# Kernel optimization log

Hardware: AMD Instinct MI355X
Metric: run time of the kernel (lower is better)

The kernel has to match this reference:

```python
import jax, jax.numpy as jnp
import numpy as np

PH = PW = 7          # pooled output size
SR = 2               # sampling_ratio: SR x SR samples per bin
SCALES = (0.25, 0.125, 0.0625, 0.03125)  # FPN strides 4,8,16,32
K = 512              # number of ROIs
B = 2                # batch (images)
IMG = 800.0


def _coords(start, bsize, P):
    # sample coords for P bins, SR samples per bin: start + p*bin + (i+0.5)*bin/SR
    j = jnp.arange(P * SR, dtype=start.dtype)
    return (start[:, None]
            + (j // SR)[None, :] * bsize[:, None]
            + ((j % SR) + 0.5)[None, :] * (bsize[:, None] / SR))  # [K, P*SR]


def _roi_align_level(feat, rois, scale):
    # feat: [B, C, H, W] ; rois: [K, 5] (batch_idx, x1, y1, x2, y2 in image coords)
    Bf, C, H, W = feat.shape
    b = rois[:, 0].astype(jnp.int32)
    x1 = rois[:, 1] * scale
    y1 = rois[:, 2] * scale
    x2 = rois[:, 3] * scale
    y2 = rois[:, 4] * scale
    roi_w = jnp.maximum(x2 - x1, 1.0)   # legacy (aligned=False) ROIAlign
    roi_h = jnp.maximum(y2 - y1, 1.0)
    ys = _coords(y1, roi_h / PH, PH)    # [K, Sy]
    xs = _coords(x1, roi_w / PW, PW)    # [K, Sx]
    y = ys[:, :, None]                  # [K, Sy, 1]
    x = xs[:, None, :]                  # [K, 1, Sx]
    valid = (y > -1.0) & (y < H) & (x > -1.0) & (x < W)  # [K, Sy, Sx]
    yc = jnp.clip(y, 0.0, None)
    xc = jnp.clip(x, 0.0, None)
    yl = jnp.minimum(yc.astype(jnp.int32), H - 1)
    xl = jnp.minimum(xc.astype(jnp.int32), W - 1)
    yh = jnp.minimum(yl + 1, H - 1)
    xh = jnp.minimum(xl + 1, W - 1)
    ly = jnp.where(yl >= H - 1, 0.0, yc - yl)
    lx = jnp.where(xl >= W - 1, 0.0, xc - xl)
    hy, hx = 1.0 - ly, 1.0 - lx
    feat_flat = feat.reshape(Bf, C, H * W)
    Sy, Sx = PH * SR, PW * SR
    acc = jnp.zeros((rois.shape[0], C, Sy, Sx), feat.dtype)
    corners = ((yl, xl, hy * hx), (yl, xh, hy * lx),
               (yh, xl, ly * hx), (yh, xh, ly * lx))
    for yy, xx, w in corners:  # fixed 4-corner loop (not a data-dim loop)
        idx = jnp.broadcast_to(yy * W + xx, (rois.shape[0], Sy, Sx))
        vals = jax.vmap(lambda bi, ii: jnp.take(feat_flat, bi, axis=0)[:, ii])(b, idx)
        acc = acc + vals * jnp.broadcast_to(w, idx.shape)[:, None, :, :]
    acc = jnp.where(valid[:, None, :, :], acc, 0.0)
    # average SRxSR samples within each 7x7 bin
    return acc.reshape(rois.shape[0], C, PH, SR, PW, SR).mean(axis=(3, 5))


def setup_inputs() -> dict:
    key = jax.random.key(0)
    ks = jax.random.split(key, 10)
    input_0 = jax.random.normal(ks[0], (B, 256, 200, 200), jnp.float32)
    input_1 = jax.random.normal(ks[1], (B, 256, 100, 100), jnp.float32)
    input_2 = jax.random.normal(ks[2], (B, 256, 50, 50), jnp.float32)
    input_3 = jax.random.normal(ks[3], (B, 256, 25, 25), jnp.float32)
    bidx = jax.random.randint(ks[4], (K,), 0, B).astype(jnp.float32)
    x1 = jax.random.uniform(ks[5], (K,)) * (IMG - 64.0)
    y1 = jax.random.uniform(ks[6], (K,)) * (IMG - 64.0)
    bw = 32.0 + jax.random.uniform(ks[7], (K,)) * 200.0
    bh = 32.0 + jax.random.uniform(ks[8], (K,)) * 200.0
    rois = jnp.stack([bidx, x1, y1,
                      jnp.minimum(x1 + bw, IMG),
                      jnp.minimum(y1 + bh, IMG)], axis=1).astype(jnp.float32)
    level = jax.random.randint(ks[9], (K,), 0, 4).astype(jnp.int32)
    rois_counts = jnp.array([K // 2, K - K // 2], jnp.int32)  # unused (all ROIs valid)
    return {"input_0": input_0, "input_1": input_1, "input_2": input_2,
            "input_3": input_3, "rois": rois, "rois_counts": rois_counts,
            "level": level}


def reference(input_0, input_1, input_2, input_3, rois, rois_counts, level):
    feats = (input_0, input_1, input_2, input_3)
    lvl = level.astype(jnp.int32)
    out = jnp.zeros((rois.shape[0], input_0.shape[1], PH, PW), input_0.dtype)
    for i, (f, s) in enumerate(zip(feats, SCALES)):
        o = _roi_align_level(f, rois, s)
        out = out + jnp.where((lvl == i)[:, None, None, None], o, 0.0)
    return out
```

## Files before the change

### kernel.cpp

```cpp
#include <hip/hip_runtime.h>


#define NUM_CH 256
#define CGRP   64
#define OFF2   5120000
#define OFF3   6400000
#define WS_FLOATS 6720000
#define TBLK_FULL 1400

typedef float floatx2 __attribute__((ext_vector_type(2)));
typedef float floatx4 __attribute__((ext_vector_type(4)));

__device__ __forceinline__ float ext4(floatx4 v, int i) {
    float r = (i == 1) ? v.y : v.x;
    r = (i == 2) ? v.z : r;
    r = (i == 3) ? v.w : r;
    return r;
}

template<int H, int W, int P>
__device__ __forceinline__ void transpose_row(
    const float* __restrict__ src, float* __restrict__ dst, int m, float* lds)
{
    int b  = m / (H * 4);
    int rm = m - b * (H * 4);
    int y  = rm >> 2;
    int ct = rm & 3;
    int tid = threadIdx.x;
    const float* s = src + (((size_t)b * NUM_CH + ct * 64) * H + y) * W;
    for (int i = tid; i < 64 * W; i += 256) {
        int c = i / W;
        int x = i - c * W;
        lds[c * P + x] = s[(size_t)c * (H * W) + x];
    }
    __syncthreads();
    float* d = dst + (((size_t)b * H + y) * (size_t)W) * NUM_CH + ct * 64;
    for (int i = tid; i < W * 64; i += 256) {
        int x = i >> 6;
        int c = i & 63;
        d[(size_t)x * NUM_CH + c] = lds[c * P + x];
    }
}

__global__ __launch_bounds__(256) void k1_transpose_gather(
    const float* __restrict__ f0,
    const float* __restrict__ f1,
    const float* __restrict__ f2,
    const float* __restrict__ f3,
    const float* __restrict__ rois_f,
    const int* __restrict__ level,
    float* __restrict__ out,
    float* __restrict__ ws,
    int K, int TBLK, int all_levels)
{
    __shared__ float lds[64 * 101];
    int bid = blockIdx.x;
    if (bid < TBLK) {
        if (bid < 800)       transpose_row<100, 100, 101>(f1, ws,        bid,        lds);
        else if (bid < 1200) transpose_row<50,  50,  51 >(f2, ws + OFF2, bid - 800,  lds);
        else                 transpose_row<25,  25,  27 >(f3, ws + OFF3, bid - 1200, lds);
        return;
    }

    int nb  = gridDim.x - TBLK;
    int lb  = bid - TBLK;
    int q   = nb >> 3, r = nb & 7;
    int xcd = lb & 7;
    int idx = lb >> 3;
    int l   = xcd * q + min(xcd, r) + idx;

    int NW  = K * CGRP;
    int wid = l * 4 + (int)(threadIdx.x >> 6);
    if (wid >= NW) return;
    int lane = threadIdx.x & 63;
    if (lane >= 49) return;

    int k  = wid % K;
    int c2 = wid / K;
    k  = __builtin_amdgcn_readfirstlane(k);
    c2 = __builtin_amdgcn_readfirstlane(c2);

    int lvl = level[k];
    if (!all_levels && lvl != 0) return;

    const float* f;
    int H, W; float scale;
    if (lvl == 0)      { f = f0; H = 200; W = 200; scale = 0.25f;    }
    else if (lvl == 1) { f = f1; H = 100; W = 100; scale = 0.125f;   }
    else if (lvl == 2) { f = f2; H = 50;  W = 50;  scale = 0.0625f;  }
    else               { f = f3; H = 25;  W = 25;  scale = 0.03125f; }

    int p  = lane;
    int ph = p / 7;
    int pw = p % 7;

    const float* rf = rois_f + (size_t)k * 5;
    float r0 = rf[0];
    float x1 = rf[1] * scale, y1 = rf[2] * scale;
    float x2 = rf[3] * scale, y2 = rf[4] * scale;
    int bi = (int)r0;
    bi = (bi < 0) ? 0 : ((bi > 1) ? 1 : bi);

    float bh = fmaxf(y2 - y1, 1.0f) * (1.0f / 7.0f);
    float bw = fmaxf(x2 - x1, 1.0f) * (1.0f / 7.0f);

    const size_t plane = (size_t)(H * W);
    const float* base  = f + ((size_t)bi * NUM_CH + c2) * plane;
    const size_t cstr  = (size_t)CGRP * plane;

    int   rA[2], rB[2];
    float lyv[2], hyv[2], vy[2];
    #pragma unroll
    for (int sy = 0; sy < 2; ++sy) {
        float y = y1 + (float)ph * bh + ((float)sy + 0.5f) * (bh * 0.5f);
        bool valid = (y > -1.0f) && (y < (float)H);
        float yc = fmaxf(y, 0.0f);
        int yl = min((int)yc, H - 1);
        int yh = min(yl + 1, H - 1);
        float ly = (yl >= H - 1) ? 0.0f : (yc - (float)yl);
        rA[sy] = yl * W;
        rB[sy] = yh * W;
        lyv[sy] = ly; hyv[sy] = 1.0f - ly;
        vy[sy] = valid ? 0.25f : 0.0f;
    }
    int   xlv[2], xhv[2];
    float lxv[2], hxv[2], vx[2];
    #pragma unroll
    for (int sx = 0; sx < 2; ++sx) {
        float x = x1 + (float)pw * bw + ((float)sx + 0.5f) * (bw * 0.5f);
        bool valid = (x > -1.0f) && (x < (float)W);
        float xc = fmaxf(x, 0.0f);
        int xl = min((int)xc, W - 1);
        float lx = (xl >= W - 1) ? 0.0f : (xc - (float)xl);
        xlv[sx] = xl;
        xhv[sx] = min(xl + 1, W - 1);
        lxv[sx] = lx; hxv[sx] = 1.0f - lx;
        vx[sx] = valid ? 1.0f : 0.0f;
    }

    float acc[4];
    #pragma unroll
    for (int j = 0; j < 4; ++j) acc[j] = 0.0f;

    if (bw <= 3.98f) {
        int xq = min(xlv[0], W - 4);
        int i0l = min(max(xlv[0] - xq, 0), 3);
        int i0h = min(max(xhv[0] - xq, 0), 3);
        int i1l = min(max(xlv[1] - xq, 0), 3);
        int i1h = min(max(xhv[1] - xq, 0), 3);

        #pragma unroll
        for (int sy = 0; sy < 2; ++sy) {
            floatx4 LA[4], LB[4];
            #pragma unroll
            for (int j = 0; j < 4; ++j) {
                const float* bj = base + (size_t)j * cstr;
                LA[j] = *(const floatx4*)(bj + rA[sy] + xq);
                LB[j] = *(const floatx4*)(bj + rB[sy] + xq);
            }
            #pragma unroll
            for (int sx = 0; sx < 2; ++sx) {
                int il = sx ? i1l : i0l;
                int ih = sx ? i1h : i0h;
                float vs  = vy[sy] * vx[sx];
                float w00 = hyv[sy] * hxv[sx] * vs;
                float w01 = hyv[sy] * lxv[sx] * vs;
                float w10 = lyv[sy] * hxv[sx] * vs;
                float w11 = lyv[sy] * lxv[sx] * vs;
                #pragma unroll
                for (int j = 0; j < 4; ++j) {
                    acc[j] += w00 * ext4(LA[j], il) + w01 * ext4(LA[j], ih)
                            + w10 * ext4(LB[j], il) + w11 * ext4(LB[j], ih);
                }
            }
        }
    } else {
        int   xb[2];
        float sel[2];
        #pragma unroll
        for (int sx = 0; sx < 2; ++sx) {
            int xq = min(xlv[sx], W - 2);
            xb[sx]  = xq;
            sel[sx] = (xlv[sx] > xq) ? 1.0f : 0.0f;
        }
        #pragma unroll
        for (int sy = 0; sy < 2; ++sy) {
            floatx2 va[4][2], vb[4][2];
            #pragma unroll
            for (int sx = 0; sx < 2; ++sx) {
                #pragma unroll
                for (int j = 0; j < 4; ++j) {
                    const float* bj = base + (size_t)j * cstr;
                    va[j][sx] = *(const floatx2*)(bj + rA[sy] + xb[sx]);
                    vb[j][sx] = *(const floatx2*)(bj + rB[sy] + xb[sx]);
                }
            }
            #pragma unroll
            for (int sx = 0; sx < 2; ++sx) {
                float vs  = vy[sy] * vx[sx];
                float w00 = hyv[sy] * hxv[sx] * vs;
                float w01 = hyv[sy] * lxv[sx] * vs;
                float w10 = lyv[sy] * hxv[sx] * vs;
                float w11 = lyv[sy] * lxv[sx] * vs;
                float s0  = sel[sx];
                #pragma unroll
                for (int j = 0; j < 4; ++j) {
                    float v00 = va[j][sx].x + s0 * (va[j][sx].y - va[j][sx].x);
                    float v10 = vb[j][sx].x + s0 * (vb[j][sx].y - vb[j][sx].x);
                    acc[j] += w00 * v00 + w01 * va[j][sx].y
                            + w10 * v10 + w11 * vb[j][sx].y;
                }
            }
        }
    }

    size_t ob = ((size_t)k * NUM_CH + c2) * 49 + p;
    #pragma unroll
    for (int j = 0; j < 4; ++j)
        out[ob + (size_t)j * (CGRP * 49)] = acc[j];
}

__global__ __launch_bounds__(256) void k2_gather_l123(
    const float* __restrict__ rois_f,
    const int* __restrict__ level,
    const float* __restrict__ ws,
    float* __restrict__ out,
    int K)
{
    __shared__ float lds[49 * 257];
    int k = blockIdx.x;
    int lvl = level[k];
    if (lvl == 0) return;

    const float* t; int H, W; float scale;
    if (lvl == 1)      { t = ws;        H = 100; W = 100; scale = 0.125f;   }
    else if (lvl == 2) { t = ws + OFF2; H = 50;  W = 50;  scale = 0.0625f;  }
    else               { t = ws + OFF3; H = 25;  W = 25;  scale = 0.03125f; }

    const float* rf = rois_f + (size_t)k * 5;
    float r0 = rf[0];
    float x1 = rf[1] * scale, y1 = rf[2] * scale;
    float x2 = rf[3] * scale, y2 = rf[4] * scale;
    int bi = (int)r0;
    bi = (bi < 0) ? 0 : ((bi > 1) ? 1 : bi);

    float bh = fmaxf(y2 - y1, 1.0f) * (1.0f / 7.0f);
    float bw = fmaxf(x2 - x1, 1.0f) * (1.0f / 7.0f);

    const float* tb = t + (size_t)bi * H * W * NUM_CH;
    int wave = threadIdx.x >> 6;
    int lane = threadIdx.x & 63;
    int cb   = lane * 4;

    for (int px = wave; px < 49; px += 4) {
        int ph = px / 7, pw = px % 7;

        int rows[4]; float lyv[2], hyv[2], vy[2];
        #pragma unroll
        for (int sy = 0; sy < 2; ++sy) {
            float y = y1 + (float)ph * bh + ((float)sy + 0.5f) * (bh * 0.5f);
            bool valid = (y > -1.0f) && (y < (float)H);
            float yc = fmaxf(y, 0.0f);
            int yl = min((int)yc, H - 1);
            int yh = min(yl + 1, H - 1);
            float ly = (yl >= H - 1) ? 0.0f : (yc - (float)yl);
            rows[2 * sy]     = yl;
            rows[2 * sy + 1] = yh;
            lyv[sy] = ly; hyv[sy] = 1.0f - ly;
            vy[sy] = valid ? 0.25f : 0.0f;
        }
        int cols[4]; float lxv[2], hxv[2], vx[2];
        #pragma unroll
        for (int sx = 0; sx < 2; ++sx) {
            float x = x1 + (float)pw * bw + ((float)sx + 0.5f) * (bw * 0.5f);
            bool valid = (x > -1.0f) && (x < (float)W);
            float xc = fmaxf(x, 0.0f);
            int xl = min((int)xc, W - 1);
            float lx = (xl >= W - 1) ? 0.0f : (xc - (float)xl);
            cols[2 * sx]     = xl;
            cols[2 * sx + 1] = min(xl + 1, W - 1);
            lxv[sx] = lx; hxv[sx] = 1.0f - lx;
            vx[sx] = valid ? 1.0f : 0.0f;
        }

        floatx4 v[4][4];
        #pragma unroll
        for (int rr = 0; rr < 4; ++rr) {
            #pragma unroll
            for (int cc = 0; cc < 4; ++cc) {
                v[rr][cc] = *(const floatx4*)(
                    tb + ((size_t)rows[rr] * W + cols[cc]) * NUM_CH + cb);
            }
        }

        floatx4 acc = {0.0f, 0.0f, 0.0f, 0.0f};
        #pragma unroll
        for (int sy = 0; sy < 2; ++sy) {
            #pragma unroll
            for (int sx = 0; sx < 2; ++sx) {
                float vs  = vy[sy] * vx[sx];
                float w00 = hyv[sy] * hxv[sx] * vs;
                float w01 = hyv[sy] * lxv[sx] * vs;
                float w10 = lyv[sy] * hxv[sx] * vs;
                float w11 = lyv[sy] * lxv[sx] * vs;
                acc += v[2 * sy][2 * sx]     * w00;
                acc += v[2 * sy][2 * sx + 1] * w01;
                acc += v[2 * sy + 1][2 * sx]     * w10;
                acc += v[2 * sy + 1][2 * sx + 1] * w11;
            }
        }

        int lb = px * 257 + cb;
        lds[lb + 0] = acc.x;
        lds[lb + 1] = acc.y;
        lds[lb + 2] = acc.z;
        lds[lb + 3] = acc.w;
    }
    __syncthreads();

    float* ob = out + (size_t)k * (NUM_CH * 49);
    for (int i = threadIdx.x; i < NUM_CH * 49; i += 256) {
        int c  = i / 49;
        int px = i - c * 49;
        ob[i] = lds[px * 257 + c];
    }
}

extern "C" void kernel_launch(void* const* d_in, const int* in_sizes, int n_in,
                              void* d_out, int out_size, void* d_ws, size_t ws_size,
                              hipStream_t stream) {
    const float* f0   = (const float*)d_in[0];
    const float* f1   = (const float*)d_in[1];
    const float* f2   = (const float*)d_in[2];
    const float* f3   = (const float*)d_in[3];
    const float* rois = (const float*)d_in[4];
    const int* level = (const int*)d_in[6];
    float* out = (float*)d_out;

    int K = out_size / (NUM_CH * 49);
    int use_ws = (ws_size >= (size_t)WS_FLOATS * 4) ? 1 : 0;
    int TBLK = use_ws ? TBLK_FULL : 0;
    int GB   = K * 16;

    k1_transpose_gather<<<TBLK + GB, 256, 0, stream>>>(
        f0, f1, f2, f3, rois, level, out, (float*)d_ws, K, TBLK, use_ws ? 0 : 1);
    if (use_ws) {
        k2_gather_l123<<<K, 256, 0, stream>>>(
            rois, level, (const float*)d_ws, out, K);
    }
}
```

Before: 192.3 us.

## Transpose level-0 features to channels-last and gather all levels from workspace

```diff
diff --git a/kernel.cpp b/kernel.cpp
--- a/kernel.cpp
+++ b/kernel.cpp
@@ -3,10 +3,13 @@
 
 #define NUM_CH 256
 #define CGRP   64
-#define OFF2   5120000
-#define OFF3   6400000
-#define WS_FLOATS 6720000
-#define TBLK_FULL 1400
+#define OFF_T2 5120000
+#define OFF_T3 6400000
+#define WS_SMALL 6720000
+#define OFF_T0 6720000
+#define WS_FULL 27200000
+#define TBLK13 1400
+#define TBLK0  3200
 
 typedef float floatx2 __attribute__((ext_vector_type(2)));
 typedef float floatx4 __attribute__((ext_vector_type(4)));
@@ -42,31 +45,202 @@
     }
 }
 
-__global__ __launch_bounds__(256) void k1_transpose_gather(
+__device__ __forceinline__ void transpose_l0(
+    const float* __restrict__ src, float* __restrict__ dst, int m, float* lds)
+{
+    int b   = m / 1600;
+    int rm  = m - b * 1600;
+    int y   = rm >> 3;
+    int sub = rm & 7;
+    int ct  = sub >> 1;
+    int xh  = sub & 1;
+    int tid = threadIdx.x;
+    const float* s = src + (((size_t)b * NUM_CH + ct * 64) * 200 + y) * 200
+                         + xh * 100;
+    for (int i = tid; i < 64 * 25; i += 256) {
+        int c  = i / 25;
+        int xq = i - c * 25;
+        floatx4 v = *(const floatx4*)(s + (size_t)c * 40000 + xq * 4);
+        float* L = lds + c * 101 + xq * 4;
+        L[0] = v.x; L[1] = v.y; L[2] = v.z; L[3] = v.w;
+    }
+    __syncthreads();
+    float* d = dst + (((size_t)b * 200 + y) * 200 + xh * 100) * (size_t)NUM_CH
+                   + ct * 64;
+    for (int i = tid; i < 100 * 16; i += 256) {
+        int x  = i >> 4;
+        int cq = (i & 15) * 4;
+        floatx4 v;
+        v.x = lds[(cq + 0) * 101 + x];
+        v.y = lds[(cq + 1) * 101 + x];
+        v.z = lds[(cq + 2) * 101 + x];
+        v.w = lds[(cq + 3) * 101 + x];
+        *(floatx4*)(d + (size_t)x * NUM_CH + cq) = v;
+    }
+}
+
+__device__ __forceinline__ void gather_roi(
+    const float* __restrict__ t, int H, int W, float scale,
+    const float* __restrict__ rf, float* __restrict__ outk, float* lds)
+{
+    float r0 = rf[0];
+    float x1 = rf[1] * scale, y1 = rf[2] * scale;
+    float x2 = rf[3] * scale, y2 = rf[4] * scale;
+    int bi = (int)r0;
+    bi = (bi < 0) ? 0 : ((bi > 1) ? 1 : bi);
+
+    float bh = fmaxf(y2 - y1, 1.0f) * (1.0f / 7.0f);
+    float bw = fmaxf(x2 - x1, 1.0f) * (1.0f / 7.0f);
+
+    const float* tb = t + (size_t)bi * H * W * NUM_CH;
+    int wave = threadIdx.x >> 6;
+    int lane = threadIdx.x & 63;
+    int cb   = lane * 4;
+
+    for (int px = wave; px < 49; px += 4) {
+        int ph = px / 7, pw = px % 7;
+
+        int rows[4]; float lyv[2], hyv[2], vy[2];
+        #pragma unroll
+        for (int sy = 0; sy < 2; ++sy) {
+            float y = y1 + (float)ph * bh + ((float)sy + 0.5f) * (bh * 0.5f);
+            bool valid = (y > -1.0f) && (y < (float)H);
+            float yc = fmaxf(y, 0.0f);
+            int yl = min((int)yc, H - 1);
+            int yh = min(yl + 1, H - 1);
+            float ly = (yl >= H - 1) ? 0.0f : (yc - (float)yl);
+            rows[2 * sy]     = yl;
+            rows[2 * sy + 1] = yh;
+            lyv[sy] = ly; hyv[sy] = 1.0f - ly;
+            vy[sy] = valid ? 0.25f : 0.0f;
+        }
+        int cols[4]; float lxv[2], hxv[2], vx[2];
+        #pragma unroll
+        for (int sx = 0; sx < 2; ++sx) {
+            float x = x1 + (float)pw * bw + ((float)sx + 0.5f) * (bw * 0.5f);
+            bool valid = (x > -1.0f) && (x < (float)W);
+            float xc = fmaxf(x, 0.0f);
+            int xl = min((int)xc, W - 1);
+            float lx = (xl >= W - 1) ? 0.0f : (xc - (float)xl);
+            cols[2 * sx]     = xl;
+            cols[2 * sx + 1] = min(xl + 1, W - 1);
+            lxv[sx] = lx; hxv[sx] = 1.0f - lx;
+            vx[sx] = valid ? 1.0f : 0.0f;
+        }
+
+        floatx4 v[4][4];
+        #pragma unroll
+        for (int rr = 0; rr < 4; ++rr) {
+            #pragma unroll
+            for (int cc = 0; cc < 4; ++cc) {
+                v[rr][cc] = *(const floatx4*)(
+                    tb + ((size_t)rows[rr] * W + cols[cc]) * NUM_CH + cb);
+            }
+        }
+
+        floatx4 acc = {0.0f, 0.0f, 0.0f, 0.0f};
+        #pragma unroll
+        for (int sy = 0; sy < 2; ++sy) {
+            #pragma unroll
+            for (int sx = 0; sx < 2; ++sx) {
+                float vs  = vy[sy] * vx[sx];
+                float w00 = hyv[sy] * hxv[sx] * vs;
+                float w01 = hyv[sy] * lxv[sx] * vs;
+                float w10 = lyv[sy] * hxv[sx] * vs;
+                float w11 = lyv[sy] * lxv[sx] * vs;
+                acc += v[2 * sy][2 * sx]         * w00;
+                acc += v[2 * sy][2 * sx + 1]     * w01;
+                acc += v[2 * sy + 1][2 * sx]     * w10;
+                acc += v[2 * sy + 1][2 * sx + 1] * w11;
+            }
+        }
+
+        int lb = px * 257 + cb;
+        lds[lb + 0] = acc.x;
+        lds[lb + 1] = acc.y;
+        lds[lb + 2] = acc.z;
+        lds[lb + 3] = acc.w;
+    }
+    __syncthreads();
+
+    for (int i = threadIdx.x; i < NUM_CH * 49; i += 256) {
+        int c  = i / 49;
+        int px = i - c * 49;
+        outk[i] = lds[px * 257 + c];
+    }
+}
+
+__global__ __launch_bounds__(256) void k_t13(
+    const float* __restrict__ f1, const float* __restrict__ f2,
+    const float* __restrict__ f3, float* __restrict__ ws)
+{
+    __shared__ float lds[64 * 101];
+    int bid = blockIdx.x;
+    if (bid < 800)       transpose_row<100, 100, 101>(f1, ws,          bid,        lds);
+    else if (bid < 1200) transpose_row<50,  50,  51 >(f2, ws + OFF_T2, bid - 800,  lds);
+    else                 transpose_row<25,  25,  27 >(f3, ws + OFF_T3, bid - 1200, lds);
+}
+
+__global__ __launch_bounds__(256) void k_t0g13(
     const float* __restrict__ f0,
-    const float* __restrict__ f1,
-    const float* __restrict__ f2,
-    const float* __restrict__ f3,
     const float* __restrict__ rois_f,
     const int* __restrict__ level,
+    float* __restrict__ ws,
     float* __restrict__ out,
-    float* __restrict__ ws,
-    int K, int TBLK, int all_levels)
+    int K)
+{
+    __shared__ float lds[49 * 257];
+    int bid = blockIdx.x;
+    if (bid < K) {
+        int k = bid;
+        int lvl = level[k];
+        if (lvl == 0) return;
+        const float* t; int H, W; float scale;
+        if (lvl == 1)      { t = ws;          H = 100; W = 100; scale = 0.125f;   }
+        else if (lvl == 2) { t = ws + OFF_T2; H = 50;  W = 50;  scale = 0.0625f;  }
+        else               { t = ws + OFF_T3; H = 25;  W = 25;  scale = 0.03125f; }
+        gather_roi(t, H, W, scale, rois_f + (size_t)k * 5,
+                   out + (size_t)k * (NUM_CH * 49), lds);
+    } else {
+        transpose_l0(f0, ws + OFF_T0, bid - K, lds);
+    }
+}
+
+__global__ __launch_bounds__(256) void k_g0(
+    const float* __restrict__ rois_f,
+    const int* __restrict__ level,
+    const float* __restrict__ ws,
+    float* __restrict__ out,
+    int K)
+{
+    __shared__ float lds[49 * 257];
+    int k = blockIdx.x;
+    if (level[k] != 0) return;
+    gather_roi(ws + OFF_T0, 200, 200, 0.25f, rois_f + (size_t)k * 5,
+               out + (size_t)k * (NUM_CH * 49), lds);
+}
+
+__global__ __launch_bounds__(256) void k1_fallback(
+    const float* __restrict__ f0, const float* __restrict__ f1,
+    const float* __restrict__ f2, const float* __restrict__ f3,
+    const float* __restrict__ rois_f, const int* __restrict__ level,
+    float* __restrict__ out, float* __restrict__ ws,
+    int K, int GB, int TBLK, int all_levels)
 {
     __shared__ float lds[64 * 101];
     int bid = blockIdx.x;
-    if (bid < TBLK) {
-        if (bid < 800)       transpose_row<100, 100, 101>(f1, ws,        bid,        lds);
-        else if (bid < 1200) transpose_row<50,  50,  51 >(f2, ws + OFF2, bid - 800,  lds);
-        else                 transpose_row<25,  25,  27 >(f3, ws + OFF3, bid - 1200, lds);
+    if (bid >= GB) {
+        int m = bid - GB;
+        if (m < 800)       transpose_row<100, 100, 101>(f1, ws,          m,        lds);
+        else if (m < 1200) transpose_row<50,  50,  51 >(f2, ws + OFF_T2, m - 800,  lds);
+        else               transpose_row<25,  25,  27 >(f3, ws + OFF_T3, m - 1200, lds);
         return;
     }
 
-    int nb  = gridDim.x - TBLK;
-    int lb  = bid - TBLK;
+    int nb  = GB;
     int q   = nb >> 3, r = nb & 7;
-    int xcd = lb & 7;
-    int idx = lb >> 3;
+    int xcd = bid & 7;
+    int idx = bid >> 3;
     int l   = xcd * q + min(xcd, r) + idx;
 
     int NW  = K * CGRP;
@@ -220,7 +394,7 @@
         out[ob + (size_t)j * (CGRP * 49)] = acc[j];
 }
 
-__global__ __launch_bounds__(256) void k2_gather_l123(
+__global__ __launch_bounds__(256) void k2_fallback(
     const float* __restrict__ rois_f,
     const int* __restrict__ level,
     const float* __restrict__ ws,
@@ -231,99 +405,12 @@
     int k = blockIdx.x;
     int lvl = level[k];
     if (lvl == 0) return;
-
     const float* t; int H, W; float scale;
-    if (lvl == 1)      { t = ws;        H = 100; W = 100; scale = 0.125f;   }
-    else if (lvl == 2) { t = ws + OFF2; H = 50;  W = 50;  scale = 0.0625f;  }
-    else               { t = ws + OFF3; H = 25;  W = 25;  scale = 0.03125f; }
-
-    const float* rf = rois_f + (size_t)k * 5;
-    float r0 = rf[0];
-    float x1 = rf[1] * scale, y1 = rf[2] * scale;
-    float x2 = rf[3] * scale, y2 = rf[4] * scale;
-    int bi = (int)r0;
-    bi = (bi < 0) ? 0 : ((bi > 1) ? 1 : bi);
-
-    float bh = fmaxf(y2 - y1, 1.0f) * (1.0f / 7.0f);
-    float bw = fmaxf(x2 - x1, 1.0f) * (1.0f / 7.0f);
-
-    const float* tb = t + (size_t)bi * H * W * NUM_CH;
-    int wave = threadIdx.x >> 6;
-    int lane = threadIdx.x & 63;
-    int cb   = lane * 4;
-
-    for (int px = wave; px < 49; px += 4) {
-        int ph = px / 7, pw = px % 7;
-
-        int rows[4]; float lyv[2], hyv[2], vy[2];
-        #pragma unroll
-        for (int sy = 0; sy < 2; ++sy) {
-            float y = y1 + (float)ph * bh + ((float)sy + 0.5f) * (bh * 0.5f);
-            bool valid = (y > -1.0f) && (y < (float)H);
-            float yc = fmaxf(y, 0.0f);
-            int yl = min((int)yc, H - 1);
-            int yh = min(yl + 1, H - 1);
-            float ly = (yl >= H - 1) ? 0.0f : (yc - (float)yl);
-            rows[2 * sy]     = yl;
-            rows[2 * sy + 1] = yh;
-            lyv[sy] = ly; hyv[sy] = 1.0f - ly;
-            vy[sy] = valid ? 0.25f : 0.0f;
-        }
-        int cols[4]; float lxv[2], hxv[2], vx[2];
-        #pragma unroll
-        for (int sx = 0; sx < 2; ++sx) {
-            float x = x1 + (float)pw * bw + ((float)sx + 0.5f) * (bw * 0.5f);
-            bool valid = (x > -1.0f) && (x < (float)W);
-            float xc = fmaxf(x, 0.0f);
-            int xl = min((int)xc, W - 1);
-            float lx = (xl >= W - 1) ? 0.0f : (xc - (float)xl);
-            cols[2 * sx]     = xl;
-            cols[2 * sx + 1] = min(xl + 1, W - 1);
-            lxv[sx] = lx; hxv[sx] = 1.0f - lx;
-            vx[sx] = valid ? 1.0f : 0.0f;
-        }
-
-        floatx4 v[4][4];
-        #pragma unroll
-        for (int rr = 0; rr < 4; ++rr) {
-            #pragma unroll
-            for (int cc = 0; cc < 4; ++cc) {
-                v[rr][cc] = *(const floatx4*)(
-                    tb + ((size_t)rows[rr] * W + cols[cc]) * NUM_CH + cb);
-            }
-        }
-
-        floatx4 acc = {0.0f, 0.0f, 0.0f, 0.0f};
-        #pragma unroll
-        for (int sy = 0; sy < 2; ++sy) {
-            #pragma unroll
-            for (int sx = 0; sx < 2; ++sx) {
-                float vs  = vy[sy] * vx[sx];
-                float w00 = hyv[sy] * hxv[sx] * vs;
-                float w01 = hyv[sy] * lxv[sx] * vs;
-                float w10 = lyv[sy] * hxv[sx] * vs;
-                float w11 = lyv[sy] * lxv[sx] * vs;
-                acc += v[2 * sy][2 * sx]     * w00;
-                acc += v[2 * sy][2 * sx + 1] * w01;
-                acc += v[2 * sy + 1][2 * sx]     * w10;
-                acc += v[2 * sy + 1][2 * sx + 1] * w11;
-            }
-        }
-
-        int lb = px * 257 + cb;
-        lds[lb + 0] = acc.x;
-        lds[lb + 1] = acc.y;
-        lds[lb + 2] = acc.z;
-        lds[lb + 3] = acc.w;
-    }
-    __syncthreads();
-
-    float* ob = out + (size_t)k * (NUM_CH * 49);
-    for (int i = threadIdx.x; i < NUM_CH * 49; i += 256) {
-        int c  = i / 49;
-        int px = i - c * 49;
-        ob[i] = lds[px * 257 + c];
-    }
+    if (lvl == 1)      { t = ws;          H = 100; W = 100; scale = 0.125f;   }
+    else if (lvl == 2) { t = ws + OFF_T2; H = 50;  W = 50;  scale = 0.0625f;  }
+    else               { t = ws + OFF_T3; H = 25;  W = 25;  scale = 0.03125f; }
+    gather_roi(t, H, W, scale, rois_f + (size_t)k * 5,
+               out + (size_t)k * (NUM_CH * 49), lds);
 }
 
 extern "C" void kernel_launch(void* const* d_in, const int* in_sizes, int n_in,
@@ -336,16 +423,22 @@
     const float* rois = (const float*)d_in[4];
     const int* level = (const int*)d_in[6];
     float* out = (float*)d_out;
+    float* ws  = (float*)d_ws;
 
     int K = out_size / (NUM_CH * 49);
-    int use_ws = (ws_size >= (size_t)WS_FLOATS * 4) ? 1 : 0;
-    int TBLK = use_ws ? TBLK_FULL : 0;
-    int GB   = K * 16;
-
-    k1_transpose_gather<<<TBLK + GB, 256, 0, stream>>>(
-        f0, f1, f2, f3, rois, level, out, (float*)d_ws, K, TBLK, use_ws ? 0 : 1);
-    if (use_ws) {
-        k2_gather_l123<<<K, 256, 0, stream>>>(
-            rois, level, (const float*)d_ws, out, K);
-    }
-}
+
+    if (ws_size >= (size_t)WS_FULL * 4) {
+        k_t13<<<TBLK13, 256, 0, stream>>>(f1, f2, f3, ws);
+        k_t0g13<<<K + TBLK0, 256, 0, stream>>>(f0, rois, level, ws, out, K);
+        k_g0<<<K, 256, 0, stream>>>(rois, level, ws, out, K);
+    } else if (ws_size >= (size_t)WS_SMALL * 4) {
+        int GB = K * 16;
+        k1_fallback<<<GB + TBLK13, 256, 0, stream>>>(
+            f0, f1, f2, f3, rois, level, out, ws, K, GB, TBLK13, 0);
+        k2_fallback<<<K, 256, 0, stream>>>(rois, level, ws, out, K);
+    } else {
+        int GB = K * 16;
+        k1_fallback<<<GB, 256, 0, stream>>>(
+            f0, f1, f2, f3, rois, level, out, ws, K, GB, 0, 1);
+    }
+}
```

Measured after the change: 222.3 us. 15.6% more time.

## Transpose level-0 features to channels-last and gather levels 1-3 directly

Applied to the files above, without the earlier changes.

```diff
diff --git a/kernel.cpp b/kernel.cpp
--- a/kernel.cpp
+++ b/kernel.cpp
@@ -3,10 +3,8 @@
 
 #define NUM_CH 256
 #define CGRP   64
-#define OFF2   5120000
-#define OFF3   6400000
-#define WS_FLOATS 6720000
-#define TBLK_FULL 1400
+#define TBLK0  3200
+#define WS_T0  20480000
 
 typedef float floatx2 __attribute__((ext_vector_type(2)));
 typedef float floatx4 __attribute__((ext_vector_type(4)));
@@ -18,31 +16,41 @@
     return r;
 }
 
-template<int H, int W, int P>
-__device__ __forceinline__ void transpose_row(
+__device__ __forceinline__ void transpose_l0(
     const float* __restrict__ src, float* __restrict__ dst, int m, float* lds)
 {
-    int b  = m / (H * 4);
-    int rm = m - b * (H * 4);
-    int y  = rm >> 2;
-    int ct = rm & 3;
+    int b   = m / 1600;
+    int rm  = m - b * 1600;
+    int y   = rm >> 3;
+    int sub = rm & 7;
+    int ct  = sub >> 1;
+    int xh  = sub & 1;
     int tid = threadIdx.x;
-    const float* s = src + (((size_t)b * NUM_CH + ct * 64) * H + y) * W;
-    for (int i = tid; i < 64 * W; i += 256) {
-        int c = i / W;
-        int x = i - c * W;
-        lds[c * P + x] = s[(size_t)c * (H * W) + x];
+    const float* s = src + (((size_t)b * NUM_CH + ct * 64) * 200 + y) * 200
+                         + xh * 100;
+    for (int i = tid; i < 64 * 25; i += 256) {
+        int c  = i / 25;
+        int xq = i - c * 25;
+        floatx4 v = *(const floatx4*)(s + (size_t)c * 40000 + xq * 4);
+        float* L = lds + c * 101 + xq * 4;
+        L[0] = v.x; L[1] = v.y; L[2] = v.z; L[3] = v.w;
     }
     __syncthreads();
-    float* d = dst + (((size_t)b * H + y) * (size_t)W) * NUM_CH + ct * 64;
-    for (int i = tid; i < W * 64; i += 256) {
-        int x = i >> 6;
-        int c = i & 63;
-        d[(size_t)x * NUM_CH + c] = lds[c * P + x];
-    }
-}
-
-__global__ __launch_bounds__(256) void k1_transpose_gather(
+    float* d = dst + (((size_t)b * 200 + y) * 200 + xh * 100) * (size_t)NUM_CH
+                   + ct * 64;
+    for (int i = tid; i < 100 * 16; i += 256) {
+        int x  = i >> 4;
+        int cq = (i & 15) * 4;
+        floatx4 v;
+        v.x = lds[(cq + 0) * 101 + x];
+        v.y = lds[(cq + 1) * 101 + x];
+        v.z = lds[(cq + 2) * 101 + x];
+        v.w = lds[(cq + 3) * 101 + x];
+        *(floatx4*)(d + (size_t)x * NUM_CH + cq) = v;
+    }
+}
+
+__global__ __launch_bounds__(256) void k_main(
     const float* __restrict__ f0,
     const float* __restrict__ f1,
     const float* __restrict__ f2,
@@ -51,19 +59,17 @@
     const int* __restrict__ level,
     float* __restrict__ out,
     float* __restrict__ ws,
-    int K, int TBLK, int all_levels)
+    int K, int tblk, int all_levels)
 {
     __shared__ float lds[64 * 101];
     int bid = blockIdx.x;
-    if (bid < TBLK) {
-        if (bid < 800)       transpose_row<100, 100, 101>(f1, ws,        bid,        lds);
-        else if (bid < 1200) transpose_row<50,  50,  51 >(f2, ws + OFF2, bid - 800,  lds);
-        else                 transpose_row<25,  25,  27 >(f3, ws + OFF3, bid - 1200, lds);
+    if (bid < tblk) {
+        transpose_l0(f0, ws, bid, lds);
         return;
     }
 
-    int nb  = gridDim.x - TBLK;
-    int lb  = bid - TBLK;
+    int lb  = bid - tblk;
+    int nb  = gridDim.x - tblk;
     int q   = nb >> 3, r = nb & 7;
     int xcd = lb & 7;
     int idx = lb >> 3;
@@ -81,7 +87,7 @@
     c2 = __builtin_amdgcn_readfirstlane(c2);
 
     int lvl = level[k];
-    if (!all_levels && lvl != 0) return;
+    if (!all_levels && lvl == 0) return;
 
     const float* f;
     int H, W; float scale;
@@ -220,7 +226,7 @@
         out[ob + (size_t)j * (CGRP * 49)] = acc[j];
 }
 
-__global__ __launch_bounds__(256) void k2_gather_l123(
+__global__ __launch_bounds__(256) void k_g0(
     const float* __restrict__ rois_f,
     const int* __restrict__ level,
     const float* __restrict__ ws,
@@ -229,13 +235,10 @@
 {
     __shared__ float lds[49 * 257];
     int k = blockIdx.x;
-    int lvl = level[k];
-    if (lvl == 0) return;
-
-    const float* t; int H, W; float scale;
-    if (lvl == 1)      { t = ws;        H = 100; W = 100; scale = 0.125f;   }
-    else if (lvl == 2) { t = ws + OFF2; H = 50;  W = 50;  scale = 0.0625f;  }
-    else               { t = ws + OFF3; H = 25;  W = 25;  scale = 0.03125f; }
+    if (level[k] != 0) return;
+
+    const int H = 200, W = 200;
+    const float scale = 0.25f;
 
     const float* rf = rois_f + (size_t)k * 5;
     float r0 = rf[0];
@@ -247,7 +250,7 @@
     float bh = fmaxf(y2 - y1, 1.0f) * (1.0f / 7.0f);
     float bw = fmaxf(x2 - x1, 1.0f) * (1.0f / 7.0f);
 
-    const float* tb = t + (size_t)bi * H * W * NUM_CH;
+    const float* tb = ws + (size_t)bi * H * W * NUM_CH;
     int wave = threadIdx.x >> 6;
     int lane = threadIdx.x & 63;
     int cb   = lane * 4;
@@ -303,8 +306,8 @@
                 float w01 = hyv[sy] * lxv[sx] * vs;
                 float w10 = lyv[sy] * hxv[sx] * vs;
                 float w11 = lyv[sy] * lxv[sx] * vs;
-                acc += v[2 * sy][2 * sx]     * w00;
-                acc += v[2 * sy][2 * sx + 1] * w01;
+                acc += v[2 * sy][2 * sx]         * w00;
+                acc += v[2 * sy][2 * sx + 1]     * w01;
                 acc += v[2 * sy + 1][2 * sx]     * w10;
                 acc += v[2 * sy + 1][2 * sx + 1] * w11;
             }
@@ -336,16 +339,17 @@
     const float* rois = (const float*)d_in[4];
     const int* level = (const int*)d_in[6];
     float* out = (float*)d_out;
-
-    int K = out_size / (NUM_CH * 49);
-    int use_ws = (ws_size >= (size_t)WS_FLOATS * 4) ? 1 : 0;
-    int TBLK = use_ws ? TBLK_FULL : 0;
-    int GB   = K * 16;
-
-    k1_transpose_gather<<<TBLK + GB, 256, 0, stream>>>(
-        f0, f1, f2, f3, rois, level, out, (float*)d_ws, K, TBLK, use_ws ? 0 : 1);
-    if (use_ws) {
-        k2_gather_l123<<<K, 256, 0, stream>>>(
-            rois, level, (const float*)d_ws, out, K);
-    }
-}
+    float* ws  = (float*)d_ws;
+
+    int K  = out_size / (NUM_CH * 49);
+    int GB = K * 16;
+
+    if (ws_size >= (size_t)WS_T0 * 4) {
+        k_main<<<TBLK0 + GB, 256, 0, stream>>>(
+            f0, f1, f2, f3, rois, level, out, ws, K, TBLK0, 0);
+        k_g0<<<K, 256, 0, stream>>>(rois, level, ws, out, K);
+    } else {
+        k_main<<<GB, 256, 0, stream>>>(
+            f0, f1, f2, f3, rois, level, out, ws, K, 0, 1);
+    }
+}
```

Measured after the change: 208.6 us. 1.08x slower.
